# Performance work log

Hardware: AMD Instinct MI355X
Metric: run time of the kernel (lower is better)

Reference implementation:

```python
import jax, jax.numpy as jnp
import numpy as np

HEADS = 6
WS = 16          # window_size
OWS = 24         # overlap_win_size
DIM = 192
TABLE = (WS + OWS - 1) ** 2  # 1521


def setup_inputs() -> dict:
    key = jax.random.key(0)
    k1, k2, k3, k4, k5, k6 = jax.random.split(key, 6)
    b = 256
    nq = WS * WS          # 256
    n = OWS * OWS         # 576
    x_q = jax.random.normal(k1, (b, nq, DIM), dtype=jnp.float32)
    x_kv = jax.random.normal(k2, (b, n, DIM), dtype=jnp.float32)
    rpi = jax.random.randint(k3, (nq, n), 0, TABLE, dtype=jnp.int64)
    Wq = jax.random.normal(k4, (DIM, DIM), dtype=jnp.float32) * 0.02
    Wkv = jax.random.normal(k5, (2 * DIM, DIM), dtype=jnp.float32) * 0.02
    bias_table = jax.random.normal(k6, (TABLE, HEADS), dtype=jnp.float32) * 0.02
    return {"x_q": x_q, "x_kv": x_kv, "rpi": rpi, "Wq": Wq, "Wkv": Wkv, "bias_table": bias_table}


def reference(x_q, x_kv, rpi, Wq, Wkv, bias_table):
    b, nq, dim = x_q.shape
    n = x_kv.shape[1]
    hd = dim // HEADS
    scale = hd ** (-0.5)

    # projections (torch Linear: y = x @ W^T)
    q = (x_q @ Wq.T).reshape(b, nq, HEADS, hd).transpose(0, 2, 1, 3)      # b h nq d
    kv = x_kv @ Wkv.T                                                    # b n 2*dim
    k, v = jnp.split(kv, 2, axis=-1)
    k = k.reshape(b, n, HEADS, hd).transpose(0, 2, 1, 3)                  # b h n d
    v = v.reshape(b, n, HEADS, hd).transpose(0, 2, 1, 3)                  # b h n d

    attn = scale * jnp.einsum('bhqd,bhkd->bhqk', q, k)                    # b h nq n

    # gathered relative-position bias: table[rpi] -> (nq, n, h)
    rpb = bias_table[rpi.reshape(-1)].reshape(nq, n, HEADS)
    # nq < n branch in source: permute(2, 0, 1) -> (h, nq, n)
    rpb = rpb.transpose(2, 0, 1)

    attn = jax.nn.softmax(attn + rpb[None], axis=-1)
    out = jnp.einsum('bhqk,bhkd->bhqd', attn, v)                          # b h nq d
    out = out.transpose(0, 2, 1, 3).reshape(b, nq, dim)
    return out
```

## Files before the change

### kernel.cpp

```cpp
#include <hip/hip_runtime.h>
#include <cstdint>

typedef unsigned short u16;
typedef short s16x8 __attribute__((ext_vector_type(8)));
typedef float f32x4 __attribute__((ext_vector_type(4)));
typedef float f32x16 __attribute__((ext_vector_type(16)));

#if __has_builtin(__builtin_amdgcn_exp2f)
#define EXP2(x) __builtin_amdgcn_exp2f(x)
#else
#define EXP2(x) __expf((x)*0.6931471805599453f)
#endif

__device__ __forceinline__ u16 f2bf(float x) {
  uint32_t u = __builtin_bit_cast(uint32_t, x);
  u += 0x7FFFu + ((u >> 16) & 1u);
  return (u16)(u >> 16);
}
__device__ __forceinline__ float bf2f(u16 v) {
  return __builtin_bit_cast(float, (uint32_t)v << 16);
}
__device__ __forceinline__ uint32_t pk_bf16(float lo, float hi) {
  uint32_t ul = __builtin_bit_cast(uint32_t, lo);
  uint32_t uh = __builtin_bit_cast(uint32_t, hi);
  ul += 0x7FFFu + ((ul >> 16) & 1u);
  uh += 0x7FFFu + ((uh >> 16) & 1u);
  return __builtin_amdgcn_perm(uh, ul, 0x07060302u);
}
__device__ __forceinline__ f32x4 mfma16(s16x8 a, s16x8 b, f32x4 c) {
  return __builtin_amdgcn_mfma_f32_16x16x32_bf16(a, b, c, 0, 0, 0);
}
__device__ __forceinline__ f32x16 mfma32(s16x8 a, s16x8 b, f32x16 c) {
  return __builtin_amdgcn_mfma_f32_32x32x16_bf16(a, b, c, 0, 0, 0);
}
__device__ __forceinline__ s16x8 ld_frag(const u16* p) {
  uint4 v = *(const uint4*)p;
  return __builtin_bit_cast(s16x8, v);
}

__global__ void prep_w(const float* __restrict__ Wq, const float* __restrict__ Wkv,
                       u16* __restrict__ wqs, u16* __restrict__ wkvs) {
  int tid = blockIdx.x * 256 + threadIdx.x;
  if (tid >= 13824) return;
  bool isQ = tid < 4608;
  int id = isQ ? tid : tid - 4608;
  int lane = id & 63, fk = id >> 6;
  int kk = fk % 6, fb = fk / 6;
  int f = fb * 16 + (lane & 15), k0 = kk * 32 + ((lane >> 4) << 3);
  const float* src = (isQ ? Wq : Wkv) + (size_t)f * 192 + k0;
  const float sc = isQ ? 0.2550348583f : 1.0f;
  float4 a = ((const float4*)src)[0], b = ((const float4*)src)[1];
  uint4 o;
  o.x = pk_bf16(a.x * sc, a.y * sc); o.y = pk_bf16(a.z * sc, a.w * sc);
  o.z = pk_bf16(b.x * sc, b.y * sc); o.w = pk_bf16(b.z * sc, b.w * sc);
  *(uint4*)&(isQ ? wqs : wkvs)[(size_t)id * 8] = o;
}

__global__ void build_rpb(const int* __restrict__ rpi, const float* __restrict__ table,
                          u16* __restrict__ rpb) {
  const int bi = blockIdx.x;
  const int h = bi / 18, kt = bi - h * 18;
  const int t = threadIdx.x, lane = t & 63, w = t >> 6;
  const int u = lane >> 5, l31 = lane & 31;
  const int q = (w << 5) + l31;
  const int n0 = (kt << 5) + (u << 2);
  u16 vals[16];
#pragma unroll
  for (int g = 0; g < 4; ++g) {
    int4 id4 = *(const int4*)&rpi[q * 576 + n0 + (g << 3)];
    vals[(g << 2) + 0] = f2bf(table[id4.x * 6 + h] * 1.4426950409f);
    vals[(g << 2) + 1] = f2bf(table[id4.y * 6 + h] * 1.4426950409f);
    vals[(g << 2) + 2] = f2bf(table[id4.z * 6 + h] * 1.4426950409f);
    vals[(g << 2) + 3] = f2bf(table[id4.w * 6 + h] * 1.4426950409f);
  }
  uint4* dst = (uint4*)&rpb[((size_t)bi * 512 + t) * 16];
  dst[0] = *(uint4*)&vals[0];
  dst[1] = *(uint4*)&vals[8];
}

template <int NC, int MODE>
__device__ __forceinline__ void proj_body(const float* __restrict__ A,
                                          const u16* __restrict__ W,
                                          u16* __restrict__ outQ, u16* __restrict__ outK,
                                          u16* __restrict__ outV, int blk,
                                          u16* __restrict__ lAf) {
  const int t = threadIdx.x, lane = t & 63, w = t >> 6, c = lane & 15, hi = lane >> 4;
  const int mbase = (blk << 6) + (w << 4);
  u16* wlds = lAf + w * 3072;
  {
    const int r = lane >> 2, cq = lane & 3;
    const float* src = A + (size_t)(mbase + r) * 192 + (cq << 2);
    const int e0 = (cq & 1) << 2;
#pragma unroll
    for (int i = 0; i < 12; ++i) {
      float4 v = *(const float4*)(src + (i << 4));
      const int kk = i >> 1, h2 = ((i & 1) << 1) + (cq >> 1);
      uint2 pv;
      pv.x = pk_bf16(v.x, v.y);
      pv.y = pk_bf16(v.z, v.w);
      *(uint2*)&wlds[(((kk << 6) + (h2 << 4) + r) << 3) + e0] = pv;
    }
  }
  asm volatile("s_waitcnt lgkmcnt(0)" ::: "memory");
  __builtin_amdgcn_sched_barrier(0);
  s16x8 af[6];
#pragma unroll
  for (int kk = 0; kk < 6; ++kk)
    af[kk] = ld_frag(&wlds[((kk << 6) + lane) << 3]);

  constexpr int TOT = NC * 6;
  const int m = mbase + c;
  s16x8 wB[3][4];
#pragma unroll
  for (int s0 = 0; s0 < 2; ++s0) {
#pragma unroll
    for (int nb = 0; nb < 4; ++nb)
      wB[s0][nb] = ld_frag(&W[((size_t)((nb * 6 + s0) * 64 + lane)) * 8]);
  }
  f32x4 acc[4];
#pragma unroll
  for (int nb = 0; nb < 4; ++nb) acc[nb] = f32x4{0.f, 0.f, 0.f, 0.f};
#pragma unroll
  for (int s = 0; s < TOT; ++s) {
    const int nc = s / 6, kk = s % 6;
    if (s + 2 < TOT) {
      const int s2 = s + 2, nc2 = s2 / 6, kk2 = s2 % 6;
#pragma unroll
      for (int nb = 0; nb < 4; ++nb)
        wB[s2 % 3][nb] = ld_frag(&W[((size_t)((((nc2 << 2) + nb) * 6 + kk2) * 64 + lane)) * 8]);
    }
#pragma unroll
    for (int nb = 0; nb < 4; ++nb)
      acc[nb] = mfma16(wB[s % 3][nb], af[kk], acc[nb]);
    if (kk == 5) {
#pragma unroll
      for (int nb = 0; nb < 4; ++nb) {
        int fb = (nc << 6) + (nb << 4) + (hi << 2);
        uint2 pv;
        pv.x = pk_bf16(acc[nb][0], acc[nb][1]);
        pv.y = pk_bf16(acc[nb][2], acc[nb][3]);
        if (MODE == 0) {
          int b = m >> 8, q = m & 255, hh = fb >> 5, d = fb & 31;
          *(uint2*)&outQ[((((size_t)(b * 6 + hh)) << 8) + q) * 32 + d] = pv;
        } else {
          int b = m / 576, tok = m - b * 576;
          if (fb >= 192) {
            int f2 = fb - 192, hh = f2 >> 5, d = f2 & 31;
            *(uint2*)&outV[(((size_t)(b * 6 + hh)) * 576 + tok) * 32 + d] = pv;
          } else {
            int hh = fb >> 5, dd = fb & 31;
            int half = dd >> 4, uu = (dd >> 3) & 1, e0 = dd & 7;
            int ktt = tok >> 5, lt = tok & 31;
            *(uint2*)&outK[(size_t)((b * 6 + hh) * 18 + ktt) * 1024 +
                           half * 512 + uu * 256 + lt * 8 + e0] = pv;
          }
        }
        acc[nb] = f32x4{0.f, 0.f, 0.f, 0.f};
      }
    }
  }
}

__launch_bounds__(256)
__global__ void proj_all(const float* __restrict__ xq, const float* __restrict__ xkv,
                         const u16* __restrict__ wqs, const u16* __restrict__ wkvs,
                         u16* __restrict__ Qws, u16* __restrict__ Kws,
                         u16* __restrict__ Vws) {
  __shared__ __align__(16) u16 lAf[12288];
  int blk = blockIdx.x;
  if (blk < 1024) proj_body<3, 0>(xq, wqs, Qws, nullptr, nullptr, blk, lAf);
  else            proj_body<6, 1>(xkv, wkvs, nullptr, Kws, Vws, blk - 1024, lAf);
}

#define VSTR 600
__launch_bounds__(512)
__global__ void attn(const u16* __restrict__ Qws, const u16* __restrict__ Kws,
                     const u16* __restrict__ Vws, const u16* __restrict__ rpb,
                     float* __restrict__ out) {
  __shared__ __align__(16) u16 Vt[32 * VSTR];
  const int bh = blockIdx.x, b = bh / 6, h = bh - b * 6;
  const size_t kvbase = (size_t)bh * 576 * 32;
  const int t = threadIdx.x;
  for (int key = t; key < 576; key += 512) {
    int kk = key & 31, k15 = kk & 15;
    int p = ((kk >> 4) << 4) | (((k15 >> 2) & 1) << 3) | ((k15 >> 3) << 2) | (k15 & 3);
    int col = ((key >> 5) << 5) + p;
    const uint4* src = (const uint4*)&Vws[kvbase + (size_t)key * 32];
    uint4 r[4] = {src[0], src[1], src[2], src[3]};
    const u16* vs = (const u16*)r;
#pragma unroll
    for (int d = 0; d < 32; ++d) Vt[d * VSTR + col] = vs[d];
  }
  const int lane = t & 63, l31 = lane & 31, u = lane >> 5, w = t >> 6;
  const int qg = (w << 5) + l31;
  s16x8 qf[2];
#pragma unroll
  for (int m = 0; m < 2; ++m)
    qf[m] = ld_frag(&Qws[((size_t)bh * 256 + qg) * 32 + (m << 4) + (u << 3)]);
  __syncthreads();
  f32x16 oacc;
#pragma unroll
  for (int r = 0; r < 16; ++r) oacc[r] = 0.f;
  float psum = 0.f;
  const u16* kfb = Kws + (size_t)bh * 18432 + (size_t)lane * 8;
  const u16* bp0 = rpb + (size_t)h * 147456 + (size_t)t * 16;
  s16x8 kA[2], kB[2];
  uint4 bA[2], bB[2];
  kA[0] = ld_frag(kfb);        kB[0] = ld_frag(kfb + 512);
  kA[1] = ld_frag(kfb + 1024); kB[1] = ld_frag(kfb + 1536);
  bA[0] = *(const uint4*)(bp0);        bB[0] = *(const uint4*)(bp0 + 8);
  bA[1] = *(const uint4*)(bp0 + 8192); bB[1] = *(const uint4*)(bp0 + 8192 + 8);
#pragma unroll 2
  for (int kt = 0; kt < 18; ++kt) {
    const int k0 = kt << 5, cur = kt & 1;
    s16x8 vf0 = ld_frag(&Vt[l31 * VSTR + k0 + (u << 3)]);
    s16x8 vf1 = ld_frag(&Vt[l31 * VSTR + k0 + 16 + (u << 3)]);
    f32x16 st;
#pragma unroll
    for (int r = 0; r < 16; ++r) st[r] = 0.f;
    st = mfma32(kA[cur], qf[0], st);
    st = mfma32(kB[cur], qf[1], st);
    uint4 bAc = bA[cur], bBc = bB[cur];
    if (kt < 16) {
      kA[cur] = ld_frag(kfb + (size_t)(kt + 2) * 1024);
      kB[cur] = ld_frag(kfb + (size_t)(kt + 2) * 1024 + 512);
      bA[cur] = *(const uint4*)(bp0 + (size_t)(kt + 2) * 8192);
      bB[cur] = *(const uint4*)(bp0 + (size_t)(kt + 2) * 8192 + 8);
    }
    const u16* b0 = (const u16*)&bAc;
    const u16* b1 = (const u16*)&bBc;
    float e[16];
#pragma unroll
    for (int r = 0; r < 8; ++r)
      e[r] = EXP2(st[r] + bf2f(b0[r]));
#pragma unroll
    for (int r = 8; r < 16; ++r)
      e[r] = EXP2(st[r] + bf2f(b1[r - 8]));
    psum += (((e[0] + e[1]) + (e[2] + e[3])) + ((e[4] + e[5]) + (e[6] + e[7]))) +
            (((e[8] + e[9]) + (e[10] + e[11])) + ((e[12] + e[13]) + (e[14] + e[15])));
    uint4 pa, pb;
    pa.x = pk_bf16(e[0], e[1]);   pa.y = pk_bf16(e[2], e[3]);
    pa.z = pk_bf16(e[4], e[5]);   pa.w = pk_bf16(e[6], e[7]);
    pb.x = pk_bf16(e[8], e[9]);   pb.y = pk_bf16(e[10], e[11]);
    pb.z = pk_bf16(e[12], e[13]); pb.w = pk_bf16(e[14], e[15]);
    s16x8 pf0 = __builtin_bit_cast(s16x8, pa);
    s16x8 pf1 = __builtin_bit_cast(s16x8, pb);
    oacc = mfma32(vf0, pf0, oacc);
    oacc = mfma32(vf1, pf1, oacc);
  }
  float tot = psum + __shfl_xor(psum, 32);
  float rs = 1.0f / tot;
  float* op = out + ((size_t)b * 256 + qg) * 192 + h * 32 + (u << 2);
#pragma unroll
  for (int g = 0; g < 4; ++g) {
    float4 o;
    o.x = oacc[(g << 2) + 0] * rs; o.y = oacc[(g << 2) + 1] * rs;
    o.z = oacc[(g << 2) + 2] * rs; o.w = oacc[(g << 2) + 3] * rs;
    *(float4*)(op + (g << 3)) = o;
  }
}

extern "C" void kernel_launch(void* const* d_in, const int* in_sizes, int n_in,
                              void* d_out, int out_size, void* d_ws, size_t ws_size,
                              hipStream_t stream) {
  const float* x_q   = (const float*)d_in[0];
  const float* x_kv  = (const float*)d_in[1];
  const int*   rpi   = (const int*)d_in[2];
  const float* Wq    = (const float*)d_in[3];
  const float* Wkv   = (const float*)d_in[4];
  const float* table = (const float*)d_in[5];
  float* out = (float*)d_out;

  char* ws = (char*)d_ws;
  u16* wqs  = (u16*)(ws);
  u16* wkvs = (u16*)(ws + 73728);
  u16* rpb  = (u16*)(ws + 221184);
  u16* Qws  = (u16*)(ws + 1990656);
  u16* Kws  = (u16*)(ws + 27156480);
  u16* Vws  = (u16*)(ws + 83779584);

  prep_w<<<54, 256, 0, stream>>>(Wq, Wkv, wqs, wkvs);
  build_rpb<<<108, 512, 0, stream>>>(rpi, table, rpb);
  proj_all<<<3328, 256, 0, stream>>>(x_q, x_kv, wqs, wkvs, Qws, Kws, Vws);
  attn<<<1536, 512, 0, stream>>>(Qws, Kws, Vws, rpb, out);
}
```

Measured before the change: 361.2 us.

## Keep projection weights resident per wave and pipeline input row tiles through LDS

```diff
diff --git a/kernel.cpp b/kernel.cpp
--- a/kernel.cpp
+++ b/kernel.cpp
@@ -78,98 +78,95 @@
   dst[1] = *(uint4*)&vals[8];
 }
 
-template <int NC, int MODE>
+template <int G, int MODE>
 __device__ __forceinline__ void proj_body(const float* __restrict__ A,
                                           const u16* __restrict__ W,
                                           u16* __restrict__ outQ, u16* __restrict__ outK,
-                                          u16* __restrict__ outV, int blk,
-                                          u16* __restrict__ lAf) {
+                                          u16* __restrict__ outV, int blk0,
+                                          u16* __restrict__ lds) {
   const int t = threadIdx.x, lane = t & 63, w = t >> 6, c = lane & 15, hi = lane >> 4;
-  const int mbase = (blk << 6) + (w << 4);
-  u16* wlds = lAf + w * 3072;
-  {
-    const int r = lane >> 2, cq = lane & 3;
-    const float* src = A + (size_t)(mbase + r) * 192 + (cq << 2);
-    const int e0 = (cq & 1) << 2;
-#pragma unroll
-    for (int i = 0; i < 12; ++i) {
-      float4 v = *(const float4*)(src + (i << 4));
-      const int kk = i >> 1, h2 = ((i & 1) << 1) + (cq >> 1);
+  s16x8 wf[G][6];
+#pragma unroll
+  for (int f = 0; f < G; ++f)
+#pragma unroll
+    for (int kk = 0; kk < 6; ++kk)
+      wf[f][kk] = ld_frag(&W[((size_t)(((w * G + f) * 6 + kk) * 64 + lane)) * 8]);
+  const int srow = t >> 4, scol = (t & 15) * 12;
+  float4 r0, r1, r2;
+  auto ISSUE = [&](int i) {
+    const float* src = A + (size_t)((blk0 * 8 + i) * 16 + srow) * 192 + scol;
+    r0 = ((const float4*)src)[0];
+    r1 = ((const float4*)src)[1];
+    r2 = ((const float4*)src)[2];
+  };
+  auto WRITE = [&](int slot) {
+    u16* sl = lds + slot * 3072;
+#pragma unroll
+    for (int j = 0; j < 3; ++j) {
+      float4 v = (j == 0) ? r0 : (j == 1) ? r1 : r2;
+      const int c0 = scol + j * 4, kk = c0 >> 5, rem = c0 & 31;
+      const int h2 = rem >> 3, e0 = rem & 7;
       uint2 pv;
       pv.x = pk_bf16(v.x, v.y);
       pv.y = pk_bf16(v.z, v.w);
-      *(uint2*)&wlds[(((kk << 6) + (h2 << 4) + r) << 3) + e0] = pv;
+      *(uint2*)&sl[((kk << 6) + (h2 << 4) + srow) * 8 + e0] = pv;
     }
-  }
-  asm volatile("s_waitcnt lgkmcnt(0)" ::: "memory");
-  __builtin_amdgcn_sched_barrier(0);
-  s16x8 af[6];
-#pragma unroll
-  for (int kk = 0; kk < 6; ++kk)
-    af[kk] = ld_frag(&wlds[((kk << 6) + lane) << 3]);
-
-  constexpr int TOT = NC * 6;
-  const int m = mbase + c;
-  s16x8 wB[3][4];
-#pragma unroll
-  for (int s0 = 0; s0 < 2; ++s0) {
-#pragma unroll
-    for (int nb = 0; nb < 4; ++nb)
-      wB[s0][nb] = ld_frag(&W[((size_t)((nb * 6 + s0) * 64 + lane)) * 8]);
-  }
-  f32x4 acc[4];
-#pragma unroll
-  for (int nb = 0; nb < 4; ++nb) acc[nb] = f32x4{0.f, 0.f, 0.f, 0.f};
-#pragma unroll
-  for (int s = 0; s < TOT; ++s) {
-    const int nc = s / 6, kk = s % 6;
-    if (s + 2 < TOT) {
-      const int s2 = s + 2, nc2 = s2 / 6, kk2 = s2 % 6;
-#pragma unroll
-      for (int nb = 0; nb < 4; ++nb)
-        wB[s2 % 3][nb] = ld_frag(&W[((size_t)((((nc2 << 2) + nb) * 6 + kk2) * 64 + lane)) * 8]);
-    }
-#pragma unroll
-    for (int nb = 0; nb < 4; ++nb)
-      acc[nb] = mfma16(wB[s % 3][nb], af[kk], acc[nb]);
-    if (kk == 5) {
-#pragma unroll
-      for (int nb = 0; nb < 4; ++nb) {
-        int fb = (nc << 6) + (nb << 4) + (hi << 2);
-        uint2 pv;
-        pv.x = pk_bf16(acc[nb][0], acc[nb][1]);
-        pv.y = pk_bf16(acc[nb][2], acc[nb][3]);
-        if (MODE == 0) {
-          int b = m >> 8, q = m & 255, hh = fb >> 5, d = fb & 31;
-          *(uint2*)&outQ[((((size_t)(b * 6 + hh)) << 8) + q) * 32 + d] = pv;
+  };
+  ISSUE(0); WRITE(0);
+  ISSUE(1);
+  for (int i = 0; i < 8; ++i) {
+    __syncthreads();
+    if (i + 1 < 8) WRITE((i + 1) % 3);
+    if (i + 2 < 8) ISSUE(i + 2);
+    const u16* sl = lds + (i % 3) * 3072;
+    s16x8 af[6];
+#pragma unroll
+    for (int kk = 0; kk < 6; ++kk)
+      af[kk] = ld_frag(&sl[((kk << 6) + lane) << 3]);
+    f32x4 acc[G];
+#pragma unroll
+    for (int f = 0; f < G; ++f) acc[f] = f32x4{0.f, 0.f, 0.f, 0.f};
+#pragma unroll
+    for (int kk = 0; kk < 6; ++kk)
+#pragma unroll
+      for (int f = 0; f < G; ++f)
+        acc[f] = mfma16(wf[f][kk], af[kk], acc[f]);
+    const int m = (blk0 * 8 + i) * 16 + c;
+#pragma unroll
+    for (int f = 0; f < G; ++f) {
+      const int fb = ((w * G + f) << 4) + (hi << 2);
+      uint2 pv;
+      pv.x = pk_bf16(acc[f][0], acc[f][1]);
+      pv.y = pk_bf16(acc[f][2], acc[f][3]);
+      if (MODE == 0) {
+        int b = m >> 8, q = m & 255, hh = fb >> 5, d = fb & 31;
+        *(uint2*)&outQ[((((size_t)(b * 6 + hh)) << 8) + q) * 32 + d] = pv;
+      } else {
+        int b = m / 576, tok = m - b * 576;
+        if (fb >= 192) {
+          int f2 = fb - 192, hh = f2 >> 5, d = f2 & 31;
+          *(uint2*)&outV[(((size_t)(b * 6 + hh)) * 576 + tok) * 32 + d] = pv;
         } else {
-          int b = m / 576, tok = m - b * 576;
-          if (fb >= 192) {
-            int f2 = fb - 192, hh = f2 >> 5, d = f2 & 31;
-            *(uint2*)&outV[(((size_t)(b * 6 + hh)) * 576 + tok) * 32 + d] = pv;
-          } else {
-            int hh = fb >> 5, dd = fb & 31;
-            int half = dd >> 4, uu = (dd >> 3) & 1, e0 = dd & 7;
-            int ktt = tok >> 5, lt = tok & 31;
-            *(uint2*)&outK[(size_t)((b * 6 + hh) * 18 + ktt) * 1024 +
-                           half * 512 + uu * 256 + lt * 8 + e0] = pv;
-          }
+          int hh = fb >> 5, dd = fb & 31;
+          int half = dd >> 4, uu = (dd >> 3) & 1, e0 = dd & 7;
+          int ktt = tok >> 5, lt = tok & 31;
+          *(uint2*)&outK[(size_t)((b * 6 + hh) * 18 + ktt) * 1024 +
+                         half * 512 + uu * 256 + lt * 8 + e0] = pv;
         }
-        acc[nb] = f32x4{0.f, 0.f, 0.f, 0.f};
       }
     }
   }
 }
 
-__launch_bounds__(256)
+__launch_bounds__(256, 2)
 __global__ void proj_all(const float* __restrict__ xq, const float* __restrict__ xkv,
                          const u16* __restrict__ wqs, const u16* __restrict__ wkvs,
                          u16* __restrict__ Qws, u16* __restrict__ Kws,
                          u16* __restrict__ Vws) {
-  __shared__ __align__(16) u16 lAf[12288];
+  __shared__ __align__(16) u16 lds[9216];
   int blk = blockIdx.x;
-  if (blk < 1024) proj_body<3, 0>(xq, wqs, Qws, nullptr, nullptr, blk, lAf);
-  else            proj_body<6, 1>(xkv, wkvs, nullptr, Kws, Vws, blk - 1024, lAf);
+  if (blk < 512) proj_body<3, 0>(xq, wqs, Qws, nullptr, nullptr, blk, lds);
+  else           proj_body<6, 1>(xkv, wkvs, nullptr, Kws, Vws, blk - 512, lds);
 }
 
 #define VSTR 600
@@ -204,15 +201,18 @@
   float psum = 0.f;
   const u16* kfb = Kws + (size_t)bh * 18432 + (size_t)lane * 8;
   const u16* bp0 = rpb + (size_t)h * 147456 + (size_t)t * 16;
-  s16x8 kA[2], kB[2];
-  uint4 bA[2], bB[2];
-  kA[0] = ld_frag(kfb);        kB[0] = ld_frag(kfb + 512);
-  kA[1] = ld_frag(kfb + 1024); kB[1] = ld_frag(kfb + 1536);
-  bA[0] = *(const uint4*)(bp0);        bB[0] = *(const uint4*)(bp0 + 8);
-  bA[1] = *(const uint4*)(bp0 + 8192); bB[1] = *(const uint4*)(bp0 + 8192 + 8);
-#pragma unroll 2
+  s16x8 kA[4], kB[4];
+  uint4 bA[4], bB[4];
+#pragma unroll
+  for (int s = 0; s < 4; ++s) {
+    kA[s] = ld_frag(kfb + (size_t)s * 1024);
+    kB[s] = ld_frag(kfb + (size_t)s * 1024 + 512);
+    bA[s] = *(const uint4*)(bp0 + (size_t)s * 8192);
+    bB[s] = *(const uint4*)(bp0 + (size_t)s * 8192 + 8);
+  }
+#pragma unroll
   for (int kt = 0; kt < 18; ++kt) {
-    const int k0 = kt << 5, cur = kt & 1;
+    const int k0 = kt << 5, cur = kt & 3;
     s16x8 vf0 = ld_frag(&Vt[l31 * VSTR + k0 + (u << 3)]);
     s16x8 vf1 = ld_frag(&Vt[l31 * VSTR + k0 + 16 + (u << 3)]);
     f32x16 st;
@@ -221,11 +221,11 @@
     st = mfma32(kA[cur], qf[0], st);
     st = mfma32(kB[cur], qf[1], st);
     uint4 bAc = bA[cur], bBc = bB[cur];
-    if (kt < 16) {
-      kA[cur] = ld_frag(kfb + (size_t)(kt + 2) * 1024);
-      kB[cur] = ld_frag(kfb + (size_t)(kt + 2) * 1024 + 512);
-      bA[cur] = *(const uint4*)(bp0 + (size_t)(kt + 2) * 8192);
-      bB[cur] = *(const uint4*)(bp0 + (size_t)(kt + 2) * 8192 + 8);
+    if (kt < 14) {
+      kA[cur] = ld_frag(kfb + (size_t)(kt + 4) * 1024);
+      kB[cur] = ld_frag(kfb + (size_t)(kt + 4) * 1024 + 512);
+      bA[cur] = *(const uint4*)(bp0 + (size_t)(kt + 4) * 8192);
+      bB[cur] = *(const uint4*)(bp0 + (size_t)(kt + 4) * 8192 + 8);
     }
     const u16* b0 = (const u16*)&bAc;
     const u16* b1 = (const u16*)&bBc;
@@ -281,6 +281,6 @@
 
   prep_w<<<54, 256, 0, stream>>>(Wq, Wkv, wqs, wkvs);
   build_rpb<<<108, 512, 0, stream>>>(rpi, table, rpb);
-  proj_all<<<3328, 256, 0, stream>>>(x_q, x_kv, wqs, wkvs, Qws, Kws, Vws);
+  proj_all<<<1664, 256, 0, stream>>>(x_q, x_kv, wqs, wkvs, Qws, Kws, Vws);
   attn<<<1536, 512, 0, stream>>>(Qws, Kws, Vws, rpb, out);
 }
```

Result: slower. 654.0 us (+81.0%).
